# Kernel optimization log

Hardware: AMD Instinct MI355X
Metric: run time of the kernel (lower is better)

## Reference

```python
import jax, jax.numpy as jnp
import numpy as np

S, NPS = 64, 48           # scenes, agents per scene
H, A = 256, 64            # edge_hidden_size, attention_dim
N = S * NPS


def setup_inputs() -> dict:
    key = jax.random.key(0)
    ks = jax.random.split(key, 6)
    spatial_ht = jax.random.normal(ks[0], (S, NPS, NPS, H), dtype=jnp.float32)
    temporal_ht = jax.random.normal(ks[1], (N, H), dtype=jnp.float32)
    ts_mask = jax.random.randint(ks[2], (N, 1), 0, 2).astype(jnp.int32)
    same_scene_mask = jnp.repeat(jnp.arange(S, dtype=jnp.int32), NPS)[:, None]
    # small init keeps exp(score) in-range (original uses raw, unstabilized exp)
    W1_w = jax.random.normal(ks[3], (A, H), dtype=jnp.float32) * 0.02
    W1_b = jnp.zeros((A,), dtype=jnp.float32)
    W2_w = jax.random.normal(ks[4], (A, H), dtype=jnp.float32) * 0.02
    W2_b = jnp.zeros((A,), dtype=jnp.float32)
    return {"spatial_ht": spatial_ht, "temporal_ht": temporal_ht,
            "W1_w": W1_w, "W1_b": W1_b, "W2_w": W2_w, "W2_b": W2_b,
            "ts_mask": ts_mask, "same_scene_mask": same_scene_mask}


def reference(spatial_ht, temporal_ht, W1_w, W1_b, W2_w, W2_b, ts_mask, same_scene_mask):
    # spatial_ht: [S, n, n, H] (stacked per-scene blocks), temporal_ht: [S*n, H]
    S_, n = spatial_ht.shape[0], spatial_ht.shape[1]
    Hd = spatial_ht.shape[-1]
    A_ = W1_w.shape[0]
    dt = spatial_ht.dtype

    m = (ts_mask[:, 0] == 1).reshape(S_, n)            # [S, n] existence mask
    ne = jnp.sum(m, axis=1).astype(dt)                  # [S] existing agents per scene

    # W1(spatial edge states), W2(temporal state of row agent i, broadcast over j)
    proj_s = jnp.einsum('snjh,ah->snja', spatial_ht, W1_w) + W1_b      # [S,n,n,A]
    t = temporal_ht.reshape(S_, n, Hd)
    proj_t = jnp.einsum('snh,ah->sna', t, W2_w) + W2_b                 # [S,n,A]

    score = jnp.einsum('snja,sna->snj', proj_s, proj_t)                # [S,n,n]
    score = score * ne[:, None, None] / jnp.sqrt(jnp.asarray(A_, dt))

    eye = jnp.eye(n, dtype=bool)
    valid = m[:, :, None] & m[:, None, :] & ~eye[None]                 # off-diag, both exist
    num = jnp.where(valid, jnp.exp(jnp.where(valid, score, 0.0)), 0.0)
    den = jnp.sum(num, axis=2, keepdims=True)                          # [S,n,1]
    attn = num / jnp.where(den > 0, den, 1.0)                          # zeros for absent rows / ne<=1 scenes

    # edge-to-node aggregation: sum_j attn[i,j] * spatial_ht[i,j,:]
    out = jnp.einsum('snjh,snj->snh', spatial_ht, attn)                # [S,n,H]
    return out.reshape(S_ * n, Hd)
```

## Files before the change

kernel.cpp:

```cpp
#include <hip/hip_runtime.h>

#define Hd 256
#define NPSd 48
#define Sd 64
#define Nd (Sd*NPSd)
#define ROWS 4

__device__ __forceinline__ void barrier_lds() {
  asm volatile("s_waitcnt lgkmcnt(0)" ::: "memory");
  __builtin_amdgcn_s_barrier();
}

template<int ENC>
__device__ __forceinline__ float dpp_ror_add(float v) {
  int t = __builtin_amdgcn_update_dpp(0, __float_as_int(v), ENC, 0xF, 0xF, true);
  return v + __int_as_float(t);
}

__global__ __launch_bounds__(256) void fused_kernel(
    const float* __restrict__ spatial,
    const float* __restrict__ temporal,
    const float* __restrict__ W1_w, const float* __restrict__ W1_b,
    const float* __restrict__ W2_w, const float* __restrict__ W2_b,
    const int* __restrict__ ts_mask,
    float* __restrict__ out) {
  __shared__ float t_lds[ROWS][4][72];
  __shared__ float pt_lds[ROWS][64];
  __shared__ float crp[4][ROWS];
  __shared__ float vred[ROWS][4][Hd];
  __shared__ float vvL[ROWS][Hd];
  __shared__ float crL[ROWS];

  int row0 = blockIdx.x * ROWS;
  int s    = row0 / NPSd;
  int i0   = row0 - s*NPSd;
  int tid  = threadIdx.x;
  int wave = tid >> 6, lane = tid & 63;
  bool bit16 = (lane & 16) != 0;
  bool bit32 = (lane & 32) != 0;

  int ml = lane < NPSd ? lane : NPSd-1;
  int mv = ts_mask[s*NPSd + ml];
  unsigned long long mb = __ballot(mv == 1 && lane < NPSd);
  int nv = __popcll(mb);
  float scale = (float)nv * 0.125f;
  int row  = row0 + wave;
  int irow = i0 + wave;
  bool rowv = ((mb >> (unsigned)irow) & 1ULL) && nv > 1;

  unsigned long long m = mb;
  int k = lane, jbit = 0, pc;
  pc = __popcll(m & 0xFFFFFFFFull); if (k >= pc) { jbit += 32; k -= pc; m >>= 32; }
  pc = __popcll(m & 0xFFFFull);     if (k >= pc) { jbit += 16; k -= pc; m >>= 16; }
  pc = __popcll(m & 0xFFull);       if (k >= pc) { jbit += 8;  k -= pc; m >>= 8; }
  pc = __popcll(m & 0xFull);        if (k >= pc) { jbit += 4;  k -= pc; m >>= 4; }
  pc = __popcll(m & 0x3ull);        if (k >= pc) { jbit += 2;  k -= pc; m >>= 2; }
  pc = (int)(m & 1ull);             if (k >= pc) { jbit += 1; }

  int al = (wave<<4) + (lane & 15);
  int q  = lane >> 4;
  float b1v = W1_b[al];
  float b2v = W2_b[al];

  {
    int r = tid >> 6, h4 = (tid & 63) << 2;
    float4 tv = *(const float4*)(temporal + (size_t)(row0 + r)*Hd + h4);
    *(float4*)&t_lds[r][h4 >> 6][h4 & 63] = tv;
  }

  float4 w2r[16];
#pragma unroll
  for (int mm = 0; mm < 16; ++mm)
    w2r[mm] = *(const float4*)(W2_w + (size_t)al*Hd + q*64 + mm*4);

  __syncthreads();

#pragma unroll
  for (int r = 0; r < ROWS; ++r) {
    float p = 0.f;
#pragma unroll
    for (int mm = 0; mm < 16; ++mm) {
      float4 wv = w2r[mm];
      p += wv.x * t_lds[r][q][mm*4+0];
      p += wv.y * t_lds[r][q][mm*4+1];
      p += wv.z * t_lds[r][q][mm*4+2];
      p += wv.w * t_lds[r][q][mm*4+3];
    }
    p += __shfl_xor(p, 16);
    p += __shfl_xor(p, 32);
    float pfull = p + b2v;
    float cb = pfull * b1v;
    cb += __shfl_xor(cb, 1);
    cb += __shfl_xor(cb, 2);
    cb += __shfl_xor(cb, 4);
    cb += __shfl_xor(cb, 8);
    if (lane < 16) pt_lds[r][(wave<<4) + lane] = pfull;
    if (lane == 0) crp[wave][r] = cb;
  }
  barrier_lds();

  float4 w1r[16];
#pragma unroll
  for (int j = 0; j < 16; ++j)
    w1r[j] = *(const float4*)(W1_w + (size_t)((wave<<4)+j)*Hd + (lane<<2));
  __builtin_amdgcn_sched_barrier(0);

  const float* rb = spatial + (size_t)row*NPSd*Hd;
  int nc = (nv + 3) >> 2;
  float4 A[4], B[4], C[4];
  int jA[4], jB[4], jC[4];

#define ISSUE(DST, JD, Ch)                                                  \
  { _Pragma("unroll")                                                       \
    for (int rr = 0; rr < 4; ++rr) {                                        \
      int slot = (Ch)*4 + rr;                                               \
      int ss = slot < nv ? slot : 0;                                        \
      int j = __builtin_amdgcn_readlane(jbit, ss);                          \
      JD[rr] = slot < nv ? j : -1;                                          \
      DST[rr] = *(const float4*)(rb + (size_t)j*Hd + (lane << 2));          \
    }                                                                       \
    __builtin_amdgcn_sched_barrier(0); }

  if (rowv) { ISSUE(A, jA, 0); }

#pragma unroll
  for (int r = 0; r < ROWS; ++r) {
    float4 v4 = make_float4(0.f,0.f,0.f,0.f);
#pragma unroll
    for (int j = 0; j < 16; ++j) {
      float pj = pt_lds[r][(wave<<4)+j];
      float4 wv = w1r[j];
      v4.x += pj*wv.x; v4.y += pj*wv.y; v4.z += pj*wv.z; v4.w += pj*wv.w;
    }
    *(float4*)&vred[r][wave][lane<<2] = v4;
  }
  barrier_lds();

#pragma unroll
  for (int r = 0; r < ROWS; ++r)
    vvL[r][tid] = vred[r][0][tid] + vred[r][1][tid]
                + vred[r][2][tid] + vred[r][3][tid];
  if (tid < ROWS)
    crL[tid] = crp[0][tid] + crp[1][tid] + crp[2][tid] + crp[3][tid];
  barrier_lds();

  float4 vv = *(const float4*)&vvL[wave][lane<<2];
  float cr = crL[wave];
  float k1 = scale * 1.44269504f;
  float k2 = cr * scale * 1.44269504f;
  float4 o4 = make_float4(0.f, 0.f, 0.f, 0.f);
  float den = 0.f;

#define DO_CHUNK(CUR, JC2)                                                  \
  { float q0 = CUR[0].x*vv.x + CUR[0].y*vv.y + CUR[0].z*vv.z + CUR[0].w*vv.w;\
    float q1 = CUR[1].x*vv.x + CUR[1].y*vv.y + CUR[1].z*vv.z + CUR[1].w*vv.w;\
    float q2 = CUR[2].x*vv.x + CUR[2].y*vv.y + CUR[2].z*vv.z + CUR[2].w*vv.w;\
    float q3 = CUR[3].x*vv.x + CUR[3].y*vv.y + CUR[3].z*vv.z + CUR[3].w*vv.w;\
    float s0 = (bit32 ? q2 : q0) + __shfl_xor((bit32 ? q0 : q2), 32);       \
    float s1 = (bit32 ? q3 : q1) + __shfl_xor((bit32 ? q1 : q3), 32);       \
    float tt = (bit16 ? s1 : s0) + __shfl_xor((bit16 ? s0 : s1), 16);       \
    tt = dpp_ror_add<0x121>(tt);                                            \
    tt = dpp_ror_add<0x122>(tt);                                            \
    tt = dpp_ror_add<0x124>(tt);                                            \
    tt = dpp_ror_add<0x128>(tt);                                            \
    int jg = bit32 ? (bit16 ? JC2[3] : JC2[2]) : (bit16 ? JC2[1] : JC2[0]); \
    bool vg = (jg >= 0) && (jg != irow);                                    \
    float nj = vg ? __builtin_exp2f(tt * k1 + k2) : 0.f;                    \
    float nB = __shfl_xor(nj, 16);                                          \
    float nC = __shfl_xor(nj, 32);                                          \
    float nD = __shfl_xor(nB, 32);                                          \
    den += (nj + nB) + (nC + nD);                                           \
    float n0 = bit32 ? (bit16 ? nD : nC) : (bit16 ? nB : nj);               \
    float n1 = bit32 ? (bit16 ? nC : nD) : (bit16 ? nj : nB);               \
    float n2 = bit32 ? (bit16 ? nB : nj) : (bit16 ? nD : nC);               \
    float n3 = bit32 ? (bit16 ? nj : nB) : (bit16 ? nC : nD);               \
    o4.x += n0*CUR[0].x; o4.y += n0*CUR[0].y; o4.z += n0*CUR[0].z; o4.w += n0*CUR[0].w; \
    o4.x += n1*CUR[1].x; o4.y += n1*CUR[1].y; o4.z += n1*CUR[1].z; o4.w += n1*CUR[1].w; \
    o4.x += n2*CUR[2].x; o4.y += n2*CUR[2].y; o4.z += n2*CUR[2].z; o4.w += n2*CUR[2].w; \
    o4.x += n3*CUR[3].x; o4.y += n3*CUR[3].y; o4.z += n3*CUR[3].z; o4.w += n3*CUR[3].w; }

  if (rowv) {
    if (nc > 1) ISSUE(B, jB, 1);
    if (nc > 2) ISSUE(C, jC, 2);
    int cc = 0;
    while (true) {
      DO_CHUNK(A, jA); if (cc + 3 < nc) ISSUE(A, jA, cc + 3);
      ++cc; if (cc >= nc) break;
      DO_CHUNK(B, jB); if (cc + 3 < nc) ISSUE(B, jB, cc + 3);
      ++cc; if (cc >= nc) break;
      DO_CHUNK(C, jC); if (cc + 3 < nc) ISSUE(C, jC, cc + 3);
      ++cc; if (cc >= nc) break;
    }
  }
#undef ISSUE
#undef DO_CHUNK

  float inv = den > 0.f ? 1.f/den : 0.f;
  o4.x *= inv; o4.y *= inv; o4.z *= inv; o4.w *= inv;
  *(float4*)(out + (size_t)row*Hd + (lane<<2)) = o4;
}

extern "C" void kernel_launch(void* const* d_in, const int* in_sizes, int n_in,
                              void* d_out, int out_size, void* d_ws, size_t ws_size,
                              hipStream_t stream) {
  const float* spatial  = (const float*)d_in[0];
  const float* temporal = (const float*)d_in[1];
  const float* W1_w     = (const float*)d_in[2];
  const float* W1_b     = (const float*)d_in[3];
  const float* W2_w     = (const float*)d_in[4];
  const float* W2_b     = (const float*)d_in[5];
  const int*   ts_mask  = (const int*)d_in[6];
  float* out = (float*)d_out;

  fused_kernel<<<Nd/ROWS, 256, 0, stream>>>(spatial, temporal, W1_w, W1_b,
                                            W2_w, W2_b, ts_mask, out);
}
```

Measured before the change: 21.20 us.

## Skip absent rows, split W1 register load, deepen spatial prefetch to four chunks

```diff
diff --git a/kernel.cpp b/kernel.cpp
--- a/kernel.cpp
+++ b/kernel.cpp
@@ -43,10 +43,16 @@
   int mv = ts_mask[s*NPSd + ml];
   unsigned long long mb = __ballot(mv == 1 && lane < NPSd);
   int nv = __popcll(mb);
-  float scale = (float)nv * 0.125f;
+  unsigned rbits = (unsigned)((mb >> (unsigned)i0) & 0xFull);
   int row  = row0 + wave;
   int irow = i0 + wave;
-  bool rowv = ((mb >> (unsigned)irow) & 1ULL) && nv > 1;
+  if (rbits == 0u || nv <= 1) {
+    float4 z = make_float4(0.f,0.f,0.f,0.f);
+    *(float4*)(out + (size_t)row*Hd + (lane<<2)) = z;
+    return;
+  }
+  float scale = (float)nv * 0.125f;
+  bool rowv = (rbits >> (unsigned)wave) & 1u;
 
   unsigned long long m = mb;
   int k = lane, jbit = 0, pc;
@@ -64,8 +70,10 @@
 
   {
     int r = tid >> 6, h4 = (tid & 63) << 2;
-    float4 tv = *(const float4*)(temporal + (size_t)(row0 + r)*Hd + h4);
-    *(float4*)&t_lds[r][h4 >> 6][h4 & 63] = tv;
+    if ((rbits >> r) & 1u) {
+      float4 tv = *(const float4*)(temporal + (size_t)(row0 + r)*Hd + h4);
+      *(float4*)&t_lds[r][h4 >> 6][h4 & 63] = tv;
+    }
   }
 
   float4 w2r[16];
@@ -77,6 +85,7 @@
 
 #pragma unroll
   for (int r = 0; r < ROWS; ++r) {
+    if (!((rbits >> r) & 1u)) continue;
     float p = 0.f;
 #pragma unroll
     for (int mm = 0; mm < 16; ++mm) {
@@ -99,16 +108,10 @@
   }
   barrier_lds();
 
-  float4 w1r[16];
-#pragma unroll
-  for (int j = 0; j < 16; ++j)
-    w1r[j] = *(const float4*)(W1_w + (size_t)((wave<<4)+j)*Hd + (lane<<2));
-  __builtin_amdgcn_sched_barrier(0);
-
   const float* rb = spatial + (size_t)row*NPSd*Hd;
   int nc = (nv + 3) >> 2;
-  float4 A[4], B[4], C[4];
-  int jA[4], jB[4], jC[4];
+  float4 A[4], B[4], C[4], D[4];
+  int jA[4], jB[4], jC[4], jD[4];
 
 #define ISSUE(DST, JD, Ch)                                                  \
   { _Pragma("unroll")                                                       \
@@ -123,23 +126,37 @@
 
   if (rowv) { ISSUE(A, jA, 0); }
 
-#pragma unroll
-  for (int r = 0; r < ROWS; ++r) {
-    float4 v4 = make_float4(0.f,0.f,0.f,0.f);
-#pragma unroll
-    for (int j = 0; j < 16; ++j) {
-      float pj = pt_lds[r][(wave<<4)+j];
-      float4 wv = w1r[j];
-      v4.x += pj*wv.x; v4.y += pj*wv.y; v4.z += pj*wv.z; v4.w += pj*wv.w;
-    }
-    *(float4*)&vred[r][wave][lane<<2] = v4;
-  }
+  float4 v4[ROWS];
+#pragma unroll
+  for (int r = 0; r < ROWS; ++r) v4[r] = make_float4(0.f,0.f,0.f,0.f);
+#pragma unroll
+  for (int jh = 0; jh < 2; ++jh) {
+    float4 w1r[8];
+#pragma unroll
+    for (int j = 0; j < 8; ++j)
+      w1r[j] = *(const float4*)(W1_w + (size_t)((wave<<4)+jh*8+j)*Hd + (lane<<2));
+#pragma unroll
+    for (int r = 0; r < ROWS; ++r) {
+      if (!((rbits >> r) & 1u)) continue;
+#pragma unroll
+      for (int j = 0; j < 8; ++j) {
+        float pj = pt_lds[r][(wave<<4)+jh*8+j];
+        float4 wv = w1r[j];
+        v4[r].x += pj*wv.x; v4[r].y += pj*wv.y;
+        v4[r].z += pj*wv.z; v4[r].w += pj*wv.w;
+      }
+    }
+  }
+#pragma unroll
+  for (int r = 0; r < ROWS; ++r)
+    if ((rbits >> r) & 1u) *(float4*)&vred[r][wave][lane<<2] = v4[r];
   barrier_lds();
 
 #pragma unroll
   for (int r = 0; r < ROWS; ++r)
-    vvL[r][tid] = vred[r][0][tid] + vred[r][1][tid]
-                + vred[r][2][tid] + vred[r][3][tid];
+    if ((rbits >> r) & 1u)
+      vvL[r][tid] = vred[r][0][tid] + vred[r][1][tid]
+                  + vred[r][2][tid] + vred[r][3][tid];
   if (tid < ROWS)
     crL[tid] = crp[0][tid] + crp[1][tid] + crp[2][tid] + crp[3][tid];
   barrier_lds();
@@ -182,13 +199,16 @@
   if (rowv) {
     if (nc > 1) ISSUE(B, jB, 1);
     if (nc > 2) ISSUE(C, jC, 2);
+    if (nc > 3) ISSUE(D, jD, 3);
     int cc = 0;
     while (true) {
-      DO_CHUNK(A, jA); if (cc + 3 < nc) ISSUE(A, jA, cc + 3);
-      ++cc; if (cc >= nc) break;
-      DO_CHUNK(B, jB); if (cc + 3 < nc) ISSUE(B, jB, cc + 3);
-      ++cc; if (cc >= nc) break;
-      DO_CHUNK(C, jC); if (cc + 3 < nc) ISSUE(C, jC, cc + 3);
+      DO_CHUNK(A, jA); if (cc + 4 < nc) ISSUE(A, jA, cc + 4);
+      ++cc; if (cc >= nc) break;
+      DO_CHUNK(B, jB); if (cc + 4 < nc) ISSUE(B, jB, cc + 4);
+      ++cc; if (cc >= nc) break;
+      DO_CHUNK(C, jC); if (cc + 4 < nc) ISSUE(C, jC, cc + 4);
+      ++cc; if (cc >= nc) break;
+      DO_CHUNK(D, jD); if (cc + 4 < nc) ISSUE(D, jD, cc + 4);
       ++cc; if (cc >= nc) break;
     }
   }
```

Result: slower. 23.89 us (+12.7%).
